# Optimization experiments

Measured on AMD Instinct MI355X. Metric: run time of the kernel, lower is better.

The kernel has to match this reference:

```python
import jax, jax.numpy as jnp
import numpy as np

Y = 1      # init kwarg y
DIM = 2    # init kwarg dim


def setup_inputs() -> dict:
    key = jax.random.key(0)
    k1, k2, k3 = jax.random.split(key, 3)
    B, L = 16, 512
    H = 32
    x = jax.random.normal(k1, (B, L, L), dtype=jnp.float32)
    # xavier_uniform-like init for weights
    lim1 = np.sqrt(6.0 / (3 + H)).astype(np.float32)
    W1 = jax.random.uniform(k2, (H, 3), dtype=jnp.float32, minval=-lim1, maxval=lim1)
    b1 = jnp.zeros((H,), dtype=jnp.float32)
    lim2 = np.sqrt(6.0 / (H + 1)).astype(np.float32)
    W2 = jax.random.uniform(k3, (1, H), dtype=jnp.float32, minval=-lim2, maxval=lim2)
    b2 = jnp.zeros((1,), dtype=jnp.float32)
    return {"x": x, "W1": W1, "b1": b1, "W2": W2, "b2": b2}


def reference(x, W1, b1, W2, b2):
    # nearest-neighbor sum along both lattice dims
    x1 = (jnp.roll(x, 1, axis=1) + jnp.roll(x, -1, axis=1)
          + jnp.roll(x, 1, axis=2) + jnp.roll(x, -1, axis=2))
    # shifted-by-y neighbor sum along DIM
    sx = jnp.roll(x, Y, axis=DIM) + jnp.roll(x, -Y, axis=DIM)
    # per-site 3-feature vector: [x^2, x1*x, sx*x] -> (B, L, L, 3)
    inp = jnp.stack([x * x, x1 * x, sx * x], axis=-1)
    # tiny pointwise MLP 3 -> 32 -> 1
    h = jnp.tanh(jnp.einsum('blmf,hf->blmh', inp, W1) + b1)
    out = jnp.einsum('blmh,oh->blmo', h, W2)[..., 0] + b2[0]
    # sum over lattice sites -> per-config scalar (B,)
    return out.sum(axis=(1, 2))
```

## Files before the change

### kernel.cpp

```cpp
#include <hip/hip_runtime.h>

#define L 512
#define LMASK 511
#define HID 32

constexpr int THREADS        = 256;
constexpr int ROWS_PER_BLOCK = 4;
constexpr int BLOCKS_PER_B   = L / ROWS_PER_BLOCK;
constexpr int NTAB           = 2048;
constexpr int GT             = 5;
constexpr int NPAIR_E        = 6;

constexpr float MAGIC   = 8388608.0f;
constexpr float CLAMPLO = 8388608.0f;
constexpr float CLAMPHI = 8396796.0f;

__global__ __launch_bounds__(THREADS)
void site_kernel(const float* __restrict__ x,
                 const float* __restrict__ W1,
                 const float* __restrict__ b1,
                 const float* __restrict__ W2,
                 float* __restrict__ partial) {
    __shared__ __align__(16) float tab_s[NTAB];
    __shared__ __align__(16) float zw_s[GT * 16];
    __shared__ __align__(16) float w2t_s[GT * 4];
    __shared__ __align__(16) float ew_s[NPAIR_E * 8];
    __shared__ __align__(8)  float ew2_s[NPAIR_E * 2];

    const int t = threadIdx.x;
    const float Ke = 2.8853900817779268f;

    if (t < HID) {
        if (t < 4 * GT) {
            const float K256 = 256.0f * Ke;
            const int g = t >> 2, q = t & 3;
            zw_s[g * 16 +  0 + q] = K256 * W1[t * 3 + 0];
            zw_s[g * 16 +  4 + q] = K256 * W1[t * 3 + 1];
            zw_s[g * 16 +  8 + q] = K256 * W1[t * 3 + 2];
            zw_s[g * 16 + 12 + q] = fmaf(K256, b1[t], 4098.0f + MAGIC);
            w2t_s[t] = -2.0f * W2[t];
        } else {
            const int e = t - 4 * GT, p = e >> 1, q = e & 1;
            ew_s[p * 8 + 0 + q] = Ke * W1[t * 3 + 0];
            ew_s[p * 8 + 2 + q] = Ke * W1[t * 3 + 1];
            ew_s[p * 8 + 4 + q] = Ke * W1[t * 3 + 2];
            ew_s[p * 8 + 6 + q] = Ke * b1[t];
            ew2_s[p * 2 + q]    = -2.0f * W2[t];
        }
    }
    for (int i = t; i < NTAB; i += THREADS) {
        const float zp = fmaf((float)i, 0.015625f, -16.001953125f);
        tab_s[i] = __builtin_amdgcn_rcpf(1.0f + __builtin_amdgcn_exp2f(zp));
    }
    __syncthreads();

    const int blk = blockIdx.x;
    const int b   = blk >> 7;
    const int i0  = (blk & (BLOCKS_PER_B - 1)) * ROWS_PER_BLOCK;
    const float* __restrict__ xb = x + (size_t)b * (L * L);

    float F0[8], F1[8], F2[8];
#pragma unroll
    for (int g = 0; g < 2; ++g) {
        const int j  = t + g * THREADS;
        const int jm = (j + LMASK) & LMASK, jp = (j + 1) & LMASK;

        float cc[6];
#pragma unroll
        for (int r = 0; r < 6; ++r) {
            const int i = (i0 + r - 1 + L) & LMASK;
            cc[r] = xb[i * L + j];
        }
#pragma unroll
        for (int s = 0; s < 4; ++s) {
            const int i   = i0 + s;
            const float lf = xb[i * L + jm];
            const float rg = xb[i * L + jp];
            const float c  = cc[s + 1];
            const float lr = lf + rg;
            const float x1 = lr + cc[s] + cc[s + 2];
            const int k = g * 4 + s;
            F0[k] = c * c;  F1[k] = x1 * c;  F2[k] = lr * c;
        }
    }

    float acc[8] = {0.f, 0.f, 0.f, 0.f, 0.f, 0.f, 0.f, 0.f};
    const char* __restrict__ tb = (const char*)tab_s;

#pragma unroll 1
    for (int gq = 0; gq < GT; ++gq) {
        const float4 wa  = *(const float4*)&zw_s[gq * 16 + 0];
        const float4 wb  = *(const float4*)&zw_s[gq * 16 + 4];
        const float4 wc  = *(const float4*)&zw_s[gq * 16 + 8];
        const float4 w0  = *(const float4*)&zw_s[gq * 16 + 12];
        const float4 w2v = *(const float4*)&w2t_s[gq * 4];
#pragma unroll
        for (int q = 0; q < 4; ++q) {
            const float waq = ((const float*)&wa)[q];
            const float wbq = ((const float*)&wb)[q];
            const float wcq = ((const float*)&wc)[q];
            const float w0q = ((const float*)&w0)[q];
            const float w2q = ((const float*)&w2v)[q];
#pragma unroll
            for (int s = 0; s < 8; ++s) {
                const float uu = fmaf(F0[s], waq, fmaf(F1[s], wbq, fmaf(F2[s], wcq, w0q)));
                const float uc = __builtin_amdgcn_fmed3f(uu, CLAMPLO, CLAMPHI);
                const int  off = __float_as_int(uc) & 0x007FFFFC;
                const float y  = *reinterpret_cast<const float*>(tb + off);
                acc[s] = fmaf(w2q, y, acc[s]);
            }
        }
    }

#pragma unroll 1
    for (int p = 0; p < NPAIR_E; ++p) {
        const float4 e0 = *(const float4*)&ew_s[p * 8 + 0];
        const float4 e1 = *(const float4*)&ew_s[p * 8 + 4];
        const float2 w2p = *(const float2*)&ew2_s[p * 2];
        const float wa0 = e0.x, wa1 = e0.y, wb0 = e0.z, wb1 = e0.w;
        const float wc0 = e1.x, wc1 = e1.y, w00 = e1.z, w01 = e1.w;
#pragma unroll
        for (int s = 0; s < 8; ++s) {
            float z0 = fmaf(F0[s], wa0, fmaf(F1[s], wb0, fmaf(F2[s], wc0, w00)));
            float z1 = fmaf(F0[s], wa1, fmaf(F1[s], wb1, fmaf(F2[s], wc1, w01)));
            z0 = __builtin_amdgcn_fmed3f(z0, -30.0f, 30.0f);
            z1 = __builtin_amdgcn_fmed3f(z1, -30.0f, 30.0f);
            const float d0 = 1.0f + __builtin_amdgcn_exp2f(z0);
            const float d1 = 1.0f + __builtin_amdgcn_exp2f(z1);
            const float nm = fmaf(w2p.x, d1, w2p.y * d0);
            const float rr = __builtin_amdgcn_rcpf(d0 * d1);
            acc[s] = fmaf(nm, rr, acc[s]);
        }
    }

    float a = ((acc[0] + acc[1]) + (acc[2] + acc[3]))
            + ((acc[4] + acc[5]) + (acc[6] + acc[7]));
#pragma unroll
    for (int off = 32; off > 0; off >>= 1)
        a += __shfl_down(a, off, 64);

    __shared__ float wsum[THREADS / 64];
    const int wid = t >> 6, lane = t & 63;
    if (lane == 0) wsum[wid] = a;
    __syncthreads();
    if (t == 0)
        partial[blk] = (wsum[0] + wsum[1]) + (wsum[2] + wsum[3]);
}

__global__ __launch_bounds__(128)
void reduce_kernel(const float* __restrict__ partial,
                   const float* __restrict__ W2,
                   const float* __restrict__ b2,
                   float* __restrict__ out) {
    const int b = blockIdx.x, t = threadIdx.x;
    const float NS = (float)(L * L);

    float v = partial[b * BLOCKS_PER_B + t];
    if (t < HID) v += NS * W2[t];
    if (t == 0)  v += NS * b2[0];

#pragma unroll
    for (int off = 32; off > 0; off >>= 1)
        v += __shfl_down(v, off, 64);

    __shared__ float ws2[2];
    if ((t & 63) == 0) ws2[t >> 6] = v;
    __syncthreads();
    if (t == 0) out[b] = ws2[0] + ws2[1];
}

extern "C" void kernel_launch(void* const* d_in, const int* in_sizes, int n_in,
                              void* d_out, int out_size, void* d_ws, size_t ws_size,
                              hipStream_t stream) {
    const float* x  = (const float*)d_in[0];
    const float* W1 = (const float*)d_in[1];
    const float* b1 = (const float*)d_in[2];
    const float* W2 = (const float*)d_in[3];
    const float* b2 = (const float*)d_in[4];
    float* out      = (float*)d_out;
    float* partial  = (float*)d_ws;

    const int B = in_sizes[0] / (L * L);

    site_kernel<<<B * BLOCKS_PER_B, THREADS, 0, stream>>>(x, W1, b1, W2, partial);
    reduce_kernel<<<B, 128, 0, stream>>>(partial, W2, b2, out);
}
```

Before: 34.09 us.

## Precompute scaled weights in prep kernel and interleave table and exp hidden units

Moves the per-block scaling of W1, b1 and W2 into a separate one-block prep kernel that writes them to workspace. The site kernel then reads them as uniform global loads, likely scalar loads, instead of going through shared memory. The fixed loops are fully unrolled so that table-lookup groups alternate with exp-based pairs, mixing LDS-bound and transcendental-bound work to improve overlap. The cost is an extra kernel launch and a larger unrolled body that may raise register pressure.

Measured after the change: 39.85 us. 16.9% more time.

```diff
diff --git a/kernel.cpp b/kernel.cpp
--- a/kernel.cpp
+++ b/kernel.cpp
@@ -15,39 +15,37 @@
 constexpr float CLAMPLO = 8388608.0f;
 constexpr float CLAMPHI = 8396796.0f;
 
+#define WGT_OFF 2048
+
+__global__ __launch_bounds__(64)
+void prep_kernel(const float* __restrict__ W1, const float* __restrict__ b1,
+                 const float* __restrict__ W2, float* __restrict__ wg) {
+    const int t = threadIdx.x;
+    const float Ke = 2.8853900817779268f;
+    if (t < 4 * GT) {
+        const float K256 = 256.0f * Ke;
+        const int g = t >> 2, q = t & 3;
+        wg[g * 16 +  0 + q] = K256 * W1[t * 3 + 0];
+        wg[g * 16 +  4 + q] = K256 * W1[t * 3 + 1];
+        wg[g * 16 +  8 + q] = K256 * W1[t * 3 + 2];
+        wg[g * 16 + 12 + q] = fmaf(K256, b1[t], 4098.0f + MAGIC);
+        wg[80 + t] = -2.0f * W2[t];
+    } else if (t < HID) {
+        const int e = t - 4 * GT, p = e >> 1, q = e & 1;
+        wg[100 + p * 8 + 0 + q] = Ke * W1[t * 3 + 0];
+        wg[100 + p * 8 + 2 + q] = Ke * W1[t * 3 + 1];
+        wg[100 + p * 8 + 4 + q] = Ke * W1[t * 3 + 2];
+        wg[100 + p * 8 + 6 + q] = Ke * b1[t];
+        wg[148 + p * 2 + q]     = -2.0f * W2[t];
+    }
+}
+
 __global__ __launch_bounds__(THREADS)
-void site_kernel(const float* __restrict__ x,
-                 const float* __restrict__ W1,
-                 const float* __restrict__ b1,
-                 const float* __restrict__ W2,
+void site_kernel(const float* __restrict__ x, const float* __restrict__ wg,
                  float* __restrict__ partial) {
     __shared__ __align__(16) float tab_s[NTAB];
-    __shared__ __align__(16) float zw_s[GT * 16];
-    __shared__ __align__(16) float w2t_s[GT * 4];
-    __shared__ __align__(16) float ew_s[NPAIR_E * 8];
-    __shared__ __align__(8)  float ew2_s[NPAIR_E * 2];
 
     const int t = threadIdx.x;
-    const float Ke = 2.8853900817779268f;
-
-    if (t < HID) {
-        if (t < 4 * GT) {
-            const float K256 = 256.0f * Ke;
-            const int g = t >> 2, q = t & 3;
-            zw_s[g * 16 +  0 + q] = K256 * W1[t * 3 + 0];
-            zw_s[g * 16 +  4 + q] = K256 * W1[t * 3 + 1];
-            zw_s[g * 16 +  8 + q] = K256 * W1[t * 3 + 2];
-            zw_s[g * 16 + 12 + q] = fmaf(K256, b1[t], 4098.0f + MAGIC);
-            w2t_s[t] = -2.0f * W2[t];
-        } else {
-            const int e = t - 4 * GT, p = e >> 1, q = e & 1;
-            ew_s[p * 8 + 0 + q] = Ke * W1[t * 3 + 0];
-            ew_s[p * 8 + 2 + q] = Ke * W1[t * 3 + 1];
-            ew_s[p * 8 + 4 + q] = Ke * W1[t * 3 + 2];
-            ew_s[p * 8 + 6 + q] = Ke * b1[t];
-            ew2_s[p * 2 + q]    = -2.0f * W2[t];
-        }
-    }
     for (int i = t; i < NTAB; i += THREADS) {
         const float zp = fmaf((float)i, 0.015625f, -16.001953125f);
         tab_s[i] = __builtin_amdgcn_rcpf(1.0f + __builtin_amdgcn_exp2f(zp));
@@ -87,20 +85,14 @@
     float acc[8] = {0.f, 0.f, 0.f, 0.f, 0.f, 0.f, 0.f, 0.f};
     const char* __restrict__ tb = (const char*)tab_s;
 
-#pragma unroll 1
-    for (int gq = 0; gq < GT; ++gq) {
-        const float4 wa  = *(const float4*)&zw_s[gq * 16 + 0];
-        const float4 wb  = *(const float4*)&zw_s[gq * 16 + 4];
-        const float4 wc  = *(const float4*)&zw_s[gq * 16 + 8];
-        const float4 w0  = *(const float4*)&zw_s[gq * 16 + 12];
-        const float4 w2v = *(const float4*)&w2t_s[gq * 4];
+    auto tgroup = [&](const int g) {
 #pragma unroll
         for (int q = 0; q < 4; ++q) {
-            const float waq = ((const float*)&wa)[q];
-            const float wbq = ((const float*)&wb)[q];
-            const float wcq = ((const float*)&wc)[q];
-            const float w0q = ((const float*)&w0)[q];
-            const float w2q = ((const float*)&w2v)[q];
+            const float waq = wg[g * 16 +  0 + q];
+            const float wbq = wg[g * 16 +  4 + q];
+            const float wcq = wg[g * 16 +  8 + q];
+            const float w0q = wg[g * 16 + 12 + q];
+            const float w2q = wg[80 + g * 4 + q];
 #pragma unroll
             for (int s = 0; s < 8; ++s) {
                 const float uu = fmaf(F0[s], waq, fmaf(F1[s], wbq, fmaf(F2[s], wcq, w0q)));
@@ -110,15 +102,13 @@
                 acc[s] = fmaf(w2q, y, acc[s]);
             }
         }
-    }
-
-#pragma unroll 1
-    for (int p = 0; p < NPAIR_E; ++p) {
-        const float4 e0 = *(const float4*)&ew_s[p * 8 + 0];
-        const float4 e1 = *(const float4*)&ew_s[p * 8 + 4];
-        const float2 w2p = *(const float2*)&ew2_s[p * 2];
-        const float wa0 = e0.x, wa1 = e0.y, wb0 = e0.z, wb1 = e0.w;
-        const float wc0 = e1.x, wc1 = e1.y, w00 = e1.z, w01 = e1.w;
+    };
+    auto epair = [&](const int p) {
+        const float wa0 = wg[100 + p * 8 + 0], wa1 = wg[100 + p * 8 + 1];
+        const float wb0 = wg[100 + p * 8 + 2], wb1 = wg[100 + p * 8 + 3];
+        const float wc0 = wg[100 + p * 8 + 4], wc1 = wg[100 + p * 8 + 5];
+        const float w00 = wg[100 + p * 8 + 6], w01 = wg[100 + p * 8 + 7];
+        const float w2x = wg[148 + p * 2 + 0], w2y = wg[148 + p * 2 + 1];
 #pragma unroll
         for (int s = 0; s < 8; ++s) {
             float z0 = fmaf(F0[s], wa0, fmaf(F1[s], wb0, fmaf(F2[s], wc0, w00)));
@@ -127,11 +117,17 @@
             z1 = __builtin_amdgcn_fmed3f(z1, -30.0f, 30.0f);
             const float d0 = 1.0f + __builtin_amdgcn_exp2f(z0);
             const float d1 = 1.0f + __builtin_amdgcn_exp2f(z1);
-            const float nm = fmaf(w2p.x, d1, w2p.y * d0);
+            const float nm = fmaf(w2x, d1, w2y * d0);
             const float rr = __builtin_amdgcn_rcpf(d0 * d1);
             acc[s] = fmaf(nm, rr, acc[s]);
         }
-    }
+    };
+
+    tgroup(0); epair(0);
+    tgroup(1); epair(1);
+    tgroup(2); epair(2);
+    tgroup(3); epair(3);
+    tgroup(4); epair(4); epair(5);
 
     float a = ((acc[0] + acc[1]) + (acc[2] + acc[3]))
             + ((acc[4] + acc[5]) + (acc[6] + acc[7]));
@@ -179,9 +175,11 @@
     const float* b2 = (const float*)d_in[4];
     float* out      = (float*)d_out;
     float* partial  = (float*)d_ws;
+    float* wg       = (float*)d_ws + WGT_OFF;
 
     const int B = in_sizes[0] / (L * L);
 
-    site_kernel<<<B * BLOCKS_PER_B, THREADS, 0, stream>>>(x, W1, b1, W2, partial);
+    prep_kernel<<<1, 64, 0, stream>>>(W1, b1, W2, wg);
+    site_kernel<<<B * BLOCKS_PER_B, THREADS, 0, stream>>>(x, wg, partial);
     reduce_kernel<<<B, 128, 0, stream>>>(partial, W2, b2, out);
 }
```
